# Kernel tuning notes

Hardware: AMD Instinct MI355X
Metric: run time of the kernel (lower is better)

## Reference

```python
import jax, jax.numpy as jnp
import numpy as np

BN_EPS = 1e-5

def gated_bottleneck(x2d, cw, cb, g, bta, mean, var, ew, eb):
    # grouped 1x1 conv: each of c1/4 groups mixes 4 adjacent channels
    N = x2d.shape[0]
    y = jnp.einsum('ngj,gj->ng', x2d.reshape(N, -1, 4), cw) + cb
    y = (y - mean) * jax.lax.rsqrt(var + BN_EPS) * g + bta  # BatchNorm1d (eval)
    y = jax.nn.gelu(y, approximate=False)
    return y @ ew.T + eb

def setup_inputs() -> dict:
    key = jax.random.key(0)
    ks = jax.random.split(key, 20)
    c1, c2, bn = 1024, 1024, 256
    d = {
        'x': jax.random.normal(ks[0], (8, 4096, c1), jnp.float32),
        'weight': jax.random.normal(ks[1], (c1, c2), jnp.float32) * (2.0 / c1) ** 0.5,
        'bias': jnp.zeros((c2,), jnp.float32),
        'cw_o': jax.random.normal(ks[2], (bn, 4), jnp.float32),
        'cb_o': jax.random.normal(ks[3], (bn,), jnp.float32),
        'bng_o': jax.random.uniform(ks[4], (bn,), jnp.float32),
        'bnb_o': jax.random.normal(ks[5], (bn,), jnp.float32),
        'bnm_o': jax.random.normal(ks[6], (bn,), jnp.float32),
        'bnv_o': jax.random.uniform(ks[7], (bn,), jnp.float32) + 0.1,
        'ew_o': jax.random.normal(ks[8], (c2, bn), jnp.float32) * 0.05,
        'eb_o': jax.random.normal(ks[9], (c2,), jnp.float32),
        'cw_i': jax.random.normal(ks[10], (bn, 4), jnp.float32),
        'cb_i': jax.random.normal(ks[11], (bn,), jnp.float32),
        'bng_i': jax.random.uniform(ks[12], (bn,), jnp.float32),
        'bnb_i': jax.random.normal(ks[13], (bn,), jnp.float32),
        'bnm_i': jax.random.normal(ks[14], (bn,), jnp.float32),
        'bnv_i': jax.random.uniform(ks[15], (bn,), jnp.float32) + 0.1,
        'ew_i': jax.random.normal(ks[16], (c1, bn), jnp.float32) * 0.05,
        'eb_i': jax.random.normal(ks[17], (c1,), jnp.float32),
        'k': 128,
        'k_in': 128,
    }
    return d

def reference(x, weight, bias, cw_o, cb_o, bng_o, bnb_o, bnm_o, bnv_o, ew_o, eb_o,
              cw_i, cb_i, bng_i, bnb_i, bnm_i, bnv_i, ew_i, eb_i, k, k_in):
    b, l, c1 = x.shape
    c2 = weight.shape[1]
    flat = x.reshape(b * l, c1)

    scores_o = jax.nn.softmax(
        gated_bottleneck(flat, cw_o, cb_o, bng_o, bnb_o, bnm_o, bnv_o, ew_o, eb_o), -1
    ).reshape(b, l, c2)
    sv_o, si_o = jax.lax.top_k(scores_o, k)          # (b,l,k)

    scores_i = jax.nn.softmax(
        gated_bottleneck(flat, cw_i, cb_i, bng_i, bnb_i, bnm_i, bnv_i, ew_i, eb_i), -1
    ).reshape(b, l, c1)
    sv_i, si_i = jax.lax.top_k(scores_i, k_in)        # (b,l,k_in)

    bi = jnp.arange(b)[:, None, None]
    li = jnp.arange(l)[None, :, None]

    # Branch A: output-sparse. einsum over gathered W columns == gather of x@W.
    y = jnp.einsum('blc,co->blo', x, weight)          # (b,l,c2)
    out_k = jnp.take_along_axis(y, si_o, axis=-1) * sv_o
    out_a = jnp.zeros((b, l, c2), x.dtype).at[bi, li, si_o].add(out_k)

    # Branch B: input-sparse. gathered-row einsum == scatter of gated x, then GEMM
    # (top-k indices are distinct so scatter-add builds the exact sparse vector).
    xg = jnp.take_along_axis(x, si_i, axis=-1) * sv_i
    xs = jnp.zeros((b, l, c1), x.dtype).at[bi, li, si_i].add(xg)
    out_b = jnp.einsum('blc,co->blo', xs, weight)

    return out_a + out_b + bias
```

## Files before the change

### kernel.cpp

```cpp
#include <hip/hip_runtime.h>
#include <hip/hip_bf16.h>

typedef __attribute__((ext_vector_type(8))) short short8;
typedef __attribute__((ext_vector_type(8))) _Float16 half8;
typedef __attribute__((ext_vector_type(4))) float f32x4;

#define NROWS 32768
#define CDIM 1024
#define BNC 256
#define TOPK 128
#define NKT 32

struct alignas(8) U4 { unsigned short x, y, z, w; };

__device__ __forceinline__ unsigned short f2bf(float f){
  union { float f; unsigned u; } v; v.f = f;
  unsigned r = v.u + 0x7FFFu + ((v.u >> 16) & 1u);
  return (unsigned short)(r >> 16);
}
__device__ __forceinline__ float bf2f(unsigned short h){
  union { unsigned u; float f; } v; v.u = ((unsigned)h) << 16;
  return v.f;
}
__device__ __forceinline__ unsigned short f2h(float f){
  _Float16 h = (_Float16)f;
  union { _Float16 h; unsigned short u; } v; v.h = h; return v.u;
}
__device__ __forceinline__ float h2f(unsigned short u){
  union { unsigned short u; _Float16 h; } v; v.u = u; return (float)v.h;
}
__device__ __forceinline__ void gl16(const void* g, void* l){
  __builtin_amdgcn_global_load_lds((const __attribute__((address_space(1))) void*)g,
                                   (__attribute__((address_space(3))) void*)l, 16, 0, 0);
}
__device__ __forceinline__ unsigned ldsaddr(const void* p){
  return (unsigned)(uintptr_t)(const __attribute__((address_space(3))) void*)p;
}
__device__ __forceinline__ short8 dsr128(unsigned addr){
  short8 r;
  asm volatile("ds_read_b128 %0, %1" : "=v"(r) : "v"(addr));
  return r;
}
__device__ __forceinline__ half8 s2h(short8 s){ union { short8 s; half8 h; } u; u.s = s; return u.h; }

__device__ __forceinline__ int swzf(int r){ return (r & 3) ^ ((r >> 2) & 1); }
__device__ __forceinline__ int swz(int o){ return o ^ (swzf(o >> 6) << 4); }

__device__ __forceinline__ void stage_tile(const unsigned short* g0, int gstride,
                                           char* lds, int tid){
  #pragma unroll
  for (int i = 0; i < 2; ++i){
    int o = tid * 16 + i * 4096;
    int lb = swz(o);
    gl16((const char*)g0 + (lb >> 6) * gstride + (lb & 63), lds + o);
  }
}
__device__ __forceinline__ int frag_off(int ridx, int lane){
  return ridx * 64 + (((lane >> 4) ^ swzf(ridx)) << 4);
}

__global__ void k_wt(const float* __restrict__ W, unsigned short* __restrict__ Wt){
  __shared__ float t[32][33];
  int tx = threadIdx.x, ty = threadIdx.y;
  int bx = blockIdx.x * 32, by = blockIdx.y * 32;
  for (int i = ty; i < 32; i += 8)
    t[i][tx] = W[(by + i) * CDIM + bx + tx];
  __syncthreads();
  for (int i = ty; i < 32; i += 8)
    Wt[(bx + i) * CDIM + by + tx] = f2bf(t[tx][i]);
}

__global__ void k_ecast(const float* __restrict__ eo, const float* __restrict__ ei,
                        unsigned short* __restrict__ ho, unsigned short* __restrict__ hi){
  int i = blockIdx.x * 256 + threadIdx.x;
  ho[i] = f2h(eo[i]);
  hi[i] = f2h(ei[i]);
}

__global__ __launch_bounds__(256) void k_bottleneck(
    const float* __restrict__ x,
    const float* __restrict__ cwo, const float* __restrict__ cbo,
    const float* __restrict__ go,  const float* __restrict__ bto,
    const float* __restrict__ mo,  const float* __restrict__ vo,
    const float* __restrict__ cwi, const float* __restrict__ cbi,
    const float* __restrict__ gi,  const float* __restrict__ bti,
    const float* __restrict__ mi,  const float* __restrict__ vi,
    unsigned short* __restrict__ xbf,
    unsigned short* __restrict__ uo, unsigned short* __restrict__ ui)
{
  const int t = threadIdx.x;
  const int r0 = blockIdx.x * 8;
  float4 cwov = ((const float4*)cwo)[t];
  float4 cwiv = ((const float4*)cwi)[t];
  float sco = go[t] * rsqrtf(vo[t] + 1e-5f);
  float sho = bto[t] - mo[t] * sco;
  float cbov = cbo[t];
  float sci = gi[t] * rsqrtf(vi[t] + 1e-5f);
  float shi = bti[t] - mi[t] * sci;
  float cbiv = cbi[t];
  for (int r = 0; r < 8; ++r){
    int row = r0 + r;
    float4 xv = ((const float4*)x)[row * 256 + t];
    U4 xb; xb.x = f2bf(xv.x); xb.y = f2bf(xv.y); xb.z = f2bf(xv.z); xb.w = f2bf(xv.w);
    ((U4*)xbf)[row * 256 + t] = xb;
    float h = xv.x*cwov.x + xv.y*cwov.y + xv.z*cwov.z + xv.w*cwov.w + cbov;
    h = h * sco + sho;
    float u = 0.5f * h * (1.0f + erff(h * 0.70710678118654752f));
    uo[row*BNC + t] = f2h(u);
    h = xv.x*cwiv.x + xv.y*cwiv.y + xv.z*cwiv.z + xv.w*cwiv.w + cbiv;
    h = h * sci + shi;
    u = 0.5f * h * (1.0f + erff(h * 0.70710678118654752f));
    ui[row*BNC + t] = f2h(u);
  }
}

__global__ __launch_bounds__(256, 3) void k_expand(
    const unsigned short* __restrict__ u16, const unsigned short* __restrict__ e16,
    const float* __restrict__ eb, unsigned short* __restrict__ Lout)
{
  __shared__ alignas(16) char lds[3 * 16384];
  const int tid = threadIdx.x;
  const int lane = tid & 63, w = tid >> 6;
  const int wr = (w >> 1) * 64, wc = (w & 1) * 64;
  int id = blockIdx.x;
  int xcd = id & 7, slot = id >> 3;
  const int row0 = (xcd * 32 + (slot >> 3)) * 128;
  const int col0 = (slot & 7) * 128;
  f32x4 acc[4][4] = {};
  auto stage = [&](int h, int buf){
    char* b = lds + buf * 16384;
    stage_tile(u16 + row0 * BNC + h * 32, 512, b, tid);
    stage_tile(e16 + col0 * BNC + h * 32, 512, b + 8192, tid);
  };
  stage(0, 0);
  stage(1, 1);
  asm volatile("s_waitcnt vmcnt(4)" ::: "memory");
  __builtin_amdgcn_s_barrier();
  const unsigned lbase = ldsaddr(lds);
  const int NK = BNC / 32;
  for (int h = 0; h < NK; ++h){
    unsigned sl = lbase + (h % 3) * 16384;
    short8 af[4], bfr[4];
    #pragma unroll
    for (int m = 0; m < 4; ++m) af[m]  = dsr128(sl + frag_off(wr + m * 16 + (lane & 15), lane));
    #pragma unroll
    for (int n = 0; n < 4; ++n) bfr[n] = dsr128(sl + 8192 + frag_off(wc + n * 16 + (lane & 15), lane));
    if (h + 2 < NK) stage(h + 2, (h + 2) % 3);
    __builtin_amdgcn_s_barrier();
    asm volatile("s_waitcnt lgkmcnt(0)" ::: "memory");
    __builtin_amdgcn_sched_barrier(0);
    __builtin_amdgcn_s_setprio(1);
    #pragma unroll
    for (int m = 0; m < 4; ++m)
      #pragma unroll
      for (int n = 0; n < 4; ++n)
        acc[m][n] = __builtin_amdgcn_mfma_f32_16x16x32_f16(s2h(af[m]), s2h(bfr[n]), acc[m][n], 0, 0, 0);
    __builtin_amdgcn_s_setprio(0);
    if (h + 2 < NK)      asm volatile("s_waitcnt vmcnt(4)" ::: "memory");
    else if (h + 1 < NK) asm volatile("s_waitcnt vmcnt(0)" ::: "memory");
    __builtin_amdgcn_s_barrier();
  }
  #pragma unroll
  for (int n = 0; n < 4; ++n){
    int col = col0 + wc + n * 16 + (lane & 15);
    float ebv = eb[col];
    #pragma unroll
    for (int m = 0; m < 4; ++m){
      int row = row0 + wr + m * 16 + ((lane >> 4) << 2);
      #pragma unroll
      for (int r = 0; r < 4; ++r)
        Lout[(size_t)(row + r) * CDIM + col] = f2h(acc[m][n][r] + ebv);
    }
  }
}

template<bool WRITE_XS>
__global__ __launch_bounds__(256) void k_select(
    const unsigned short* __restrict__ Lg, const unsigned short* __restrict__ xg,
    unsigned short* __restrict__ obf)
{
  const int lane = threadIdx.x & 63;
  const int wv = threadIdx.x >> 6;
  int id = blockIdx.x;
  int xcd = id & 7, rest = id >> 3;
  int q = rest >> 5, b = rest & 31;
  const int row = (xcd * 32 + q) * 128 + b * 4 + wv;
  const unsigned short* Lr = Lg + (size_t)row * CDIM;
  unsigned short hv[16];
  #pragma unroll
  for (int c = 0; c < 2; ++c){
    short8 t8 = ((const short8*)Lr)[c * 64 + lane];
    #pragma unroll
    for (int j = 0; j < 8; ++j) hv[c*8+j] = (unsigned short)t8[j];
  }
  unsigned kx[16];
  #pragma unroll
  for (int j = 0; j < 16; ++j){
    unsigned u = hv[j];
    kx[j] = u ^ ((u & 0x8000u) ? 0xFFFFu : 0x8000u);
  }
  float v[16];
  #pragma unroll
  for (int j = 0; j < 16; ++j) v[j] = h2f(hv[j]);
  float M = v[0];
  #pragma unroll
  for (int j = 1; j < 16; ++j) M = fmaxf(M, v[j]);
  #pragma unroll
  for (int off = 32; off > 0; off >>= 1) M = fmaxf(M, __shfl_xor(M, off));
  float e[16];
  float S = 0.f;
  #pragma unroll
  for (int j = 0; j < 16; ++j){ e[j] = expf(v[j] - M); S += e[j]; }
  #pragma unroll
  for (int off = 32; off > 0; off >>= 1) S += __shfl_xor(S, off);
  unsigned pref = 0;
  for (int bit = 15; bit >= 0; --bit){
    unsigned cand = pref | (1u << bit);
    int c = 0;
    #pragma unroll
    for (int j = 0; j < 16; ++j)
      c += (int)__popcll(__ballot(kx[j] >= cand));
    if (c >= TOPK) pref = cand;
  }
  float invS = 1.0f / S;
  #pragma unroll
  for (int c = 0; c < 2; ++c){
    unsigned short o8[8];
    #pragma unroll
    for (int j = 0; j < 8; ++j){
      int jj = c*8 + j;
      float sc = (kx[jj] >= pref) ? e[jj] * invS : 0.f;
      o8[j] = f2bf(sc);
    }
    if (WRITE_XS){
      short8 xv = ((const short8*)(xg + (size_t)row * CDIM))[c * 64 + lane];
      #pragma unroll
      for (int j = 0; j < 8; ++j){
        float sc = bf2f(o8[j]);
        int jj = c*8 + j;
        float scf = (kx[jj] >= pref) ? e[jj] * invS : 0.f;
        (void)sc;
        o8[j] = f2bf(bf2f((unsigned short)xv[j]) * scf);
      }
    }
    short8 st;
    #pragma unroll
    for (int j = 0; j < 8; ++j) st[j] = (short)o8[j];
    ((short8*)(obf + (size_t)row * CDIM))[c * 64 + lane] = st;
  }
}

__global__ __launch_bounds__(256, 2) void k_main(
    const unsigned short* __restrict__ xbf, const unsigned short* __restrict__ xsbf,
    const unsigned short* __restrict__ wt,  const unsigned short* __restrict__ sobf,
    const float* __restrict__ bias, float* __restrict__ out)
{
  __shared__ alignas(16) char lds[3 * 24576];
  const int tid = threadIdx.x;
  const int lane = tid & 63, w = tid >> 6;
  const int wr = (w >> 1) * 64, wc = (w & 1) * 64;
  int id = blockIdx.x;
  int xcd = id & 7, sl = id >> 3;
  const int row0 = (xcd * 32 + (sl >> 3)) * 128;
  const int col0 = (sl & 7) * 128;
  f32x4 acc1[4][4] = {}, acc2[4][4] = {};
  auto stage = [&](int kt, int buf){
    char* b = lds + buf * 24576;
    stage_tile(xbf  + row0 * CDIM + kt * 32, 2048, b, tid);
    stage_tile(xsbf + row0 * CDIM + kt * 32, 2048, b + 8192, tid);
    stage_tile(wt   + col0 * CDIM + kt * 32, 2048, b + 16384, tid);
  };
  stage(0, 0);
  stage(1, 1);
  asm volatile("s_waitcnt vmcnt(6)" ::: "memory");
  __builtin_amdgcn_s_barrier();
  const unsigned lbase = ldsaddr(lds);
  for (int kt = 0; kt < NKT; ++kt){
    const unsigned slr = lbase + (kt % 3) * 24576;
    short8 a1f[4], a2f[4], bfr[4];
    #pragma unroll
    for (int m = 0; m < 4; ++m){
      int fo = frag_off(wr + m * 16 + (lane & 15), lane);
      a1f[m] = dsr128(slr + fo);
      a2f[m] = dsr128(slr + 8192 + fo);
    }
    #pragma unroll
    for (int n = 0; n < 4; ++n)
      bfr[n] = dsr128(slr + 16384 + frag_off(wc + n * 16 + (lane & 15), lane));
    if (kt + 2 < NKT) stage(kt + 2, (kt + 2) % 3);
    asm volatile("s_waitcnt lgkmcnt(0)" ::: "memory");
    __builtin_amdgcn_sched_barrier(0);
    __builtin_amdgcn_s_setprio(1);
    #pragma unroll
    for (int m = 0; m < 4; ++m)
      #pragma unroll
      for (int n = 0; n < 4; ++n){
        acc1[m][n] = __builtin_amdgcn_mfma_f32_16x16x32_bf16(a1f[m], bfr[n], acc1[m][n], 0, 0, 0);
        acc2[m][n] = __builtin_amdgcn_mfma_f32_16x16x32_bf16(a2f[m], bfr[n], acc2[m][n], 0, 0, 0);
      }
    __builtin_amdgcn_s_setprio(0);
    if (kt + 2 < NKT)      asm volatile("s_waitcnt vmcnt(6)" ::: "memory");
    else if (kt + 1 < NKT) asm volatile("s_waitcnt vmcnt(0)" ::: "memory");
    __builtin_amdgcn_s_barrier();
  }
  #pragma unroll
  for (int n = 0; n < 4; ++n){
    int col = col0 + wc + n * 16 + (lane & 15);
    float bv = bias[col];
    #pragma unroll
    for (int m = 0; m < 4; ++m){
      int row = row0 + wr + m * 16 + ((lane >> 4) << 2);
      #pragma unroll
      for (int r = 0; r < 4; ++r){
        float so = bf2f(sobf[(size_t)(row + r) * CDIM + col]);
        out[(size_t)(row + r) * CDIM + col] = acc1[m][n][r] * so + acc2[m][n][r] + bv;
      }
    }
  }
}

extern "C" void kernel_launch(void* const* d_in, const int* in_sizes, int n_in,
                              void* d_out, int out_size, void* d_ws, size_t ws_size,
                              hipStream_t stream)
{
  const float* x    = (const float*)d_in[0];
  const float* W    = (const float*)d_in[1];
  const float* bias = (const float*)d_in[2];
  const float* cwo  = (const float*)d_in[3];
  const float* cbo  = (const float*)d_in[4];
  const float* bngo = (const float*)d_in[5];
  const float* bnbo = (const float*)d_in[6];
  const float* bnmo = (const float*)d_in[7];
  const float* bnvo = (const float*)d_in[8];
  const float* ewo  = (const float*)d_in[9];
  const float* ebo  = (const float*)d_in[10];
  const float* cwi  = (const float*)d_in[11];
  const float* cbi  = (const float*)d_in[12];
  const float* bngi = (const float*)d_in[13];
  const float* bnbi = (const float*)d_in[14];
  const float* bnmi = (const float*)d_in[15];
  const float* bnvi = (const float*)d_in[16];
  const float* ewi  = (const float*)d_in[17];
  const float* ebi  = (const float*)d_in[18];
  float* out = (float*)d_out;
  (void)in_sizes; (void)n_in; (void)out_size; (void)ws_size;

  char* ws = (char*)d_ws;
  size_t off = 0;
  auto alloc = [&](size_t bytes){ void* p = ws + off; off += (bytes + 255) & ~(size_t)255; return p; };
  unsigned short* xbf  = (unsigned short*)alloc((size_t)NROWS * CDIM * 2);
  unsigned short* xsbf = (unsigned short*)alloc((size_t)NROWS * CDIM * 2);
  unsigned short* sobf = (unsigned short*)alloc((size_t)NROWS * CDIM * 2);
  unsigned short* Lbuf = (unsigned short*)alloc((size_t)NROWS * CDIM * 2);
  unsigned short* uo   = (unsigned short*)alloc((size_t)NROWS * BNC * 2);
  unsigned short* ui   = (unsigned short*)alloc((size_t)NROWS * BNC * 2);
  unsigned short* wtb  = (unsigned short*)alloc((size_t)CDIM * CDIM * 2);
  unsigned short* e16o = (unsigned short*)alloc((size_t)CDIM * BNC * 2);
  unsigned short* e16i = (unsigned short*)alloc((size_t)CDIM * BNC * 2);

  k_wt<<<dim3(32, 32), dim3(32, 8), 0, stream>>>(W, wtb);
  k_ecast<<<dim3(1024), dim3(256), 0, stream>>>(ewo, ewi, e16o, e16i);
  k_bottleneck<<<dim3(NROWS / 8), dim3(256), 0, stream>>>(
      x, cwo, cbo, bngo, bnbo, bnmo, bnvo,
      cwi, cbi, bngi, bnbi, bnmi, bnvi, xbf, uo, ui);
  k_expand<<<dim3(2048), dim3(256), 0, stream>>>(uo, e16o, ebo, Lbuf);
  k_select<false><<<dim3(NROWS / 4), dim3(256), 0, stream>>>(Lbuf, nullptr, sobf);
  k_expand<<<dim3(2048), dim3(256), 0, stream>>>(ui, e16i, ebi, Lbuf);
  k_select<true><<<dim3(NROWS / 4), dim3(256), 0, stream>>>(Lbuf, xbf, xsbf);
  k_main<<<dim3(2048), dim3(256), 0, stream>>>(xbf, xsbf, wtb, sobf, bias, out);
}
```

Baseline: 369.2 us.

## Switch GEMM operands to fp16 and load A fragments directly from global memory

Changes the bf16 storage of x, the sparse x, the output scores and the transposed W to fp16, and uses f16 MFMA in the main GEMM. In k_main, the two A operands are no longer staged through LDS. Each lane loads its fragments straight from global memory into registers, double-buffered across iterations, and only the W tile goes through a smaller three-slot LDS ring. This is meant to cut LDS traffic and footprint, which could raise occupancy. The cost is uncoalesced 16-byte global loads for A with no reuse across waves, and fp16 can overflow where bf16 would not.

New measurement: 503.6 us. 36.4% more time.

```diff
diff --git a/kernel.cpp b/kernel.cpp
--- a/kernel.cpp
+++ b/kernel.cpp
@@ -67,7 +67,7 @@
     t[i][tx] = W[(by + i) * CDIM + bx + tx];
   __syncthreads();
   for (int i = ty; i < 32; i += 8)
-    Wt[(bx + i) * CDIM + by + tx] = f2bf(t[tx][i]);
+    Wt[(bx + i) * CDIM + by + tx] = f2h(t[tx][i]);
 }
 
 __global__ void k_ecast(const float* __restrict__ eo, const float* __restrict__ ei,
@@ -85,7 +85,7 @@
     const float* __restrict__ cwi, const float* __restrict__ cbi,
     const float* __restrict__ gi,  const float* __restrict__ bti,
     const float* __restrict__ mi,  const float* __restrict__ vi,
-    unsigned short* __restrict__ xbf,
+    unsigned short* __restrict__ x16,
     unsigned short* __restrict__ uo, unsigned short* __restrict__ ui)
 {
   const int t = threadIdx.x;
@@ -101,8 +101,8 @@
   for (int r = 0; r < 8; ++r){
     int row = r0 + r;
     float4 xv = ((const float4*)x)[row * 256 + t];
-    U4 xb; xb.x = f2bf(xv.x); xb.y = f2bf(xv.y); xb.z = f2bf(xv.z); xb.w = f2bf(xv.w);
-    ((U4*)xbf)[row * 256 + t] = xb;
+    U4 xb; xb.x = f2h(xv.x); xb.y = f2h(xv.y); xb.z = f2h(xv.z); xb.w = f2h(xv.w);
+    ((U4*)x16)[row * 256 + t] = xb;
     float h = xv.x*cwov.x + xv.y*cwov.y + xv.z*cwov.z + xv.w*cwov.w + cbov;
     h = h * sco + sho;
     float u = 0.5f * h * (1.0f + erff(h * 0.70710678118654752f));
@@ -226,21 +226,20 @@
   #pragma unroll
   for (int c = 0; c < 2; ++c){
     unsigned short o8[8];
-    #pragma unroll
-    for (int j = 0; j < 8; ++j){
-      int jj = c*8 + j;
-      float sc = (kx[jj] >= pref) ? e[jj] * invS : 0.f;
-      o8[j] = f2bf(sc);
-    }
     if (WRITE_XS){
       short8 xv = ((const short8*)(xg + (size_t)row * CDIM))[c * 64 + lane];
       #pragma unroll
       for (int j = 0; j < 8; ++j){
-        float sc = bf2f(o8[j]);
         int jj = c*8 + j;
         float scf = (kx[jj] >= pref) ? e[jj] * invS : 0.f;
-        (void)sc;
-        o8[j] = f2bf(bf2f((unsigned short)xv[j]) * scf);
+        o8[j] = f2h(h2f((unsigned short)xv[j]) * scf);
+      }
+    } else {
+      #pragma unroll
+      for (int j = 0; j < 8; ++j){
+        int jj = c*8 + j;
+        float sc = (kx[jj] >= pref) ? e[jj] * invS : 0.f;
+        o8[j] = f2h(sc);
       }
     }
     short8 st;
@@ -251,11 +250,11 @@
 }
 
 __global__ __launch_bounds__(256, 2) void k_main(
-    const unsigned short* __restrict__ xbf, const unsigned short* __restrict__ xsbf,
-    const unsigned short* __restrict__ wt,  const unsigned short* __restrict__ sobf,
+    const unsigned short* __restrict__ x16, const unsigned short* __restrict__ xs16,
+    const unsigned short* __restrict__ wt,  const unsigned short* __restrict__ so16,
     const float* __restrict__ bias, float* __restrict__ out)
 {
-  __shared__ alignas(16) char lds[3 * 24576];
+  __shared__ alignas(16) char lds[3 * 8192];
   const int tid = threadIdx.x;
   const int lane = tid & 63, w = tid >> 6;
   const int wr = (w >> 1) * 64, wc = (w & 1) * 64;
@@ -264,30 +263,38 @@
   const int row0 = (xcd * 32 + (sl >> 3)) * 128;
   const int col0 = (sl & 7) * 128;
   f32x4 acc1[4][4] = {}, acc2[4][4] = {};
-  auto stage = [&](int kt, int buf){
-    char* b = lds + buf * 24576;
-    stage_tile(xbf  + row0 * CDIM + kt * 32, 2048, b, tid);
-    stage_tile(xsbf + row0 * CDIM + kt * 32, 2048, b + 8192, tid);
-    stage_tile(wt   + col0 * CDIM + kt * 32, 2048, b + 16384, tid);
+  const unsigned lbase = ldsaddr(lds);
+
+  auto stageB = [&](int kt){
+    char* slot = lds + (kt % 3) * 8192;
+    stage_tile(wt + col0 * CDIM + kt * 32, 2048, slot, tid);
   };
-  stage(0, 0);
-  stage(1, 1);
-  asm volatile("s_waitcnt vmcnt(6)" ::: "memory");
+  auto loadA = [&](int kt, short8 (&d1)[4], short8 (&d2)[4]){
+    #pragma unroll
+    for (int m = 0; m < 4; ++m){
+      size_t o = (size_t)(row0 + wr + m * 16 + (lane & 15)) * CDIM
+               + (size_t)kt * 32 + ((lane >> 4) << 3);
+      d1[m] = *(const short8*)(x16 + o);
+      d2[m] = *(const short8*)(xs16 + o);
+    }
+  };
+
+  short8 aA1[4], aA2[4], aB1[4], aB2[4];
+  loadA(0, aA1, aA2);
+  stageB(0);
+  stageB(1);
+  asm volatile("s_waitcnt vmcnt(2)" ::: "memory");
   __builtin_amdgcn_s_barrier();
-  const unsigned lbase = ldsaddr(lds);
-  for (int kt = 0; kt < NKT; ++kt){
-    const unsigned slr = lbase + (kt % 3) * 24576;
-    short8 a1f[4], a2f[4], bfr[4];
-    #pragma unroll
-    for (int m = 0; m < 4; ++m){
-      int fo = frag_off(wr + m * 16 + (lane & 15), lane);
-      a1f[m] = dsr128(slr + fo);
-      a2f[m] = dsr128(slr + 8192 + fo);
-    }
+
+  auto body = [&](int kt, short8 (&c1)[4], short8 (&c2)[4],
+                  short8 (&n1)[4], short8 (&n2)[4]){
+    const unsigned slr = lbase + (kt % 3) * 8192;
+    short8 bfr[4];
     #pragma unroll
     for (int n = 0; n < 4; ++n)
-      bfr[n] = dsr128(slr + 16384 + frag_off(wc + n * 16 + (lane & 15), lane));
-    if (kt + 2 < NKT) stage(kt + 2, (kt + 2) % 3);
+      bfr[n] = dsr128(slr + frag_off(wc + n * 16 + (lane & 15), lane));
+    if (kt + 1 < NKT) loadA(kt + 1, n1, n2);
+    if (kt + 2 < NKT) stageB(kt + 2);
     asm volatile("s_waitcnt lgkmcnt(0)" ::: "memory");
     __builtin_amdgcn_sched_barrier(0);
     __builtin_amdgcn_s_setprio(1);
@@ -295,14 +302,20 @@
     for (int m = 0; m < 4; ++m)
       #pragma unroll
       for (int n = 0; n < 4; ++n){
-        acc1[m][n] = __builtin_amdgcn_mfma_f32_16x16x32_bf16(a1f[m], bfr[n], acc1[m][n], 0, 0, 0);
-        acc2[m][n] = __builtin_amdgcn_mfma_f32_16x16x32_bf16(a2f[m], bfr[n], acc2[m][n], 0, 0, 0);
+        acc1[m][n] = __builtin_amdgcn_mfma_f32_16x16x32_f16(s2h(c1[m]), s2h(bfr[n]), acc1[m][n], 0, 0, 0);
+        acc2[m][n] = __builtin_amdgcn_mfma_f32_16x16x32_f16(s2h(c2[m]), s2h(bfr[n]), acc2[m][n], 0, 0, 0);
       }
     __builtin_amdgcn_s_setprio(0);
-    if (kt + 2 < NKT)      asm volatile("s_waitcnt vmcnt(6)" ::: "memory");
+    if (kt + 2 < NKT)      asm volatile("s_waitcnt vmcnt(2)" ::: "memory");
     else if (kt + 1 < NKT) asm volatile("s_waitcnt vmcnt(0)" ::: "memory");
     __builtin_amdgcn_s_barrier();
-  }
+  };
+
+  for (int kt = 0; kt < NKT; kt += 2){
+    body(kt,     aA1, aA2, aB1, aB2);
+    body(kt + 1, aB1, aB2, aA1, aA2);
+  }
+
   #pragma unroll
   for (int n = 0; n < 4; ++n){
     int col = col0 + wc + n * 16 + (lane & 15);
@@ -312,7 +325,7 @@
       int row = row0 + wr + m * 16 + ((lane >> 4) << 2);
       #pragma unroll
       for (int r = 0; r < 4; ++r){
-        float so = bf2f(sobf[(size_t)(row + r) * CDIM + col]);
+        float so = h2f(so16[(size_t)(row + r) * CDIM + col]);
         out[(size_t)(row + r) * CDIM + col] = acc1[m][n][r] * so + acc2[m][n][r] + bv;
       }
     }
@@ -348,9 +361,9 @@
   char* ws = (char*)d_ws;
   size_t off = 0;
   auto alloc = [&](size_t bytes){ void* p = ws + off; off += (bytes + 255) & ~(size_t)255; return p; };
-  unsigned short* xbf  = (unsigned short*)alloc((size_t)NROWS * CDIM * 2);
-  unsigned short* xsbf = (unsigned short*)alloc((size_t)NROWS * CDIM * 2);
-  unsigned short* sobf = (unsigned short*)alloc((size_t)NROWS * CDIM * 2);
+  unsigned short* x16  = (unsigned short*)alloc((size_t)NROWS * CDIM * 2);
+  unsigned short* xs16 = (unsigned short*)alloc((size_t)NROWS * CDIM * 2);
+  unsigned short* so16 = (unsigned short*)alloc((size_t)NROWS * CDIM * 2);
   unsigned short* Lbuf = (unsigned short*)alloc((size_t)NROWS * CDIM * 2);
   unsigned short* uo   = (unsigned short*)alloc((size_t)NROWS * BNC * 2);
   unsigned short* ui   = (unsigned short*)alloc((size_t)NROWS * BNC * 2);
@@ -362,10 +375,10 @@
   k_ecast<<<dim3(1024), dim3(256), 0, stream>>>(ewo, ewi, e16o, e16i);
   k_bottleneck<<<dim3(NROWS / 8), dim3(256), 0, stream>>>(
       x, cwo, cbo, bngo, bnbo, bnmo, bnvo,
-      cwi, cbi, bngi, bnbi, bnmi, bnvi, xbf, uo, ui);
+      cwi, cbi, bngi, bnbi, bnmi, bnvi, x16, uo, ui);
   k_expand<<<dim3(2048), dim3(256), 0, stream>>>(uo, e16o, ebo, Lbuf);
-  k_select<false><<<dim3(NROWS / 4), dim3(256), 0, stream>>>(Lbuf, nullptr, sobf);
+  k_select<false><<<dim3(NROWS / 4), dim3(256), 0, stream>>>(Lbuf, nullptr, so16);
   k_expand<<<dim3(2048), dim3(256), 0, stream>>>(ui, e16i, ebi, Lbuf);
-  k_select<true><<<dim3(NROWS / 4), dim3(256), 0, stream>>>(Lbuf, xbf, xsbf);
-  k_main<<<dim3(2048), dim3(256), 0, stream>>>(xbf, xsbf, wtb, sobf, bias, out);
-}
+  k_select<true><<<dim3(NROWS / 4), dim3(256), 0, stream>>>(Lbuf, x16, xs16);
+  k_main<<<dim3(2048), dim3(256), 0, stream>>>(x16, xs16, wtb, so16, bias, out);
+}
```
